# Kernel optimization log

Measured on AMD Instinct MI355X. Metric: run time of the kernel, lower is better.

## Reference

```python
import jax, jax.numpy as jnp
import numpy as np

N_NODES = 65536
N_EDGES = 524288
IN_CH = 128
HEADS = 4
HID = 16          # per-head channels (hidden_channels)
HC = HEADS * HID  # 64
EDGE_F = 8
N_GRAPHS = 512


def _glorot(key, shape):
    return jax.random.normal(key, shape, dtype=jnp.float32) / np.float32(np.sqrt(shape[0]))


def setup_inputs() -> dict:
    key = jax.random.key(0)
    ks = jax.random.split(key, 16)
    inp = {}
    inp['x'] = jax.random.normal(ks[0], (N_NODES, IN_CH), jnp.float32)
    inp['edge_attr'] = jax.random.normal(ks[1], (N_EDGES, EDGE_F), jnp.float32)
    inp['edge_index'] = jax.random.randint(ks[2], (2, N_EDGES), 0, N_NODES, dtype=jnp.int32)
    inp['batch'] = jnp.sort(jax.random.randint(ks[3], (N_NODES,), 0, N_GRAPHS, dtype=jnp.int32))
    fan1 = {'Wq1': IN_CH, 'Wk1': IN_CH, 'Wv1': IN_CH, 'We1': EDGE_F, 'Ws1': IN_CH}
    fan2 = {'Wq2': HC, 'Wk2': HC, 'Wv2': HC, 'We2': EDGE_F, 'Ws2': HC}
    i = 4
    for name, fi in {**fan1, **fan2}.items():
        inp[name] = _glorot(ks[i], (fi, HC)); i += 1
    for b in ['bq1', 'bk1', 'bv1', 'be1', 'bs1', 'bq2', 'bk2', 'bv2', 'be2', 'bs2']:
        inp[b] = jnp.zeros((HC,), jnp.float32)
    return inp


def _tconv(x, src, dst, ea, Wq, Wk, Wv, We, Ws, bq, bk, bv, be, bs):
    """PyG TransformerConv (concat=True, root_weight=True), eval mode (no dropout)."""
    n = x.shape[0]
    q = (x @ Wq + bq).reshape(n, HEADS, HID)[dst]      # [E,H,C] query at target
    k = (x @ Wk + bk).reshape(n, HEADS, HID)[src]      # [E,H,C] key from source
    v = (x @ Wv + bv).reshape(n, HEADS, HID)[src]      # [E,H,C]
    e = (ea @ We + be).reshape(-1, HEADS, HID)         # [E,H,C] edge proj
    k = k + e
    logits = (q * k).sum(-1) / np.float32(np.sqrt(HID))  # [E,H]
    m = jax.ops.segment_max(logits, dst, num_segments=n)
    m = jnp.where(jnp.isfinite(m), m, jnp.zeros_like(m))
    a = jnp.exp(logits - m[dst])
    denom = jax.ops.segment_sum(a, dst, num_segments=n)
    alpha = a / jnp.maximum(denom[dst], 1e-16)         # segment softmax over incoming edges
    msg = (v + e) * alpha[..., None]                   # [E,H,C]
    out = jax.ops.segment_sum(msg, dst, num_segments=n).reshape(n, HC)
    return out + x @ Ws + bs                           # root/skip connection


def reference(x, edge_attr, Wq1, Wk1, Wv1, We1, Ws1, bq1, bk1, bv1, be1, bs1,
              Wq2, Wk2, Wv2, We2, Ws2, bq2, bk2, bv2, be2, bs2,
              edge_index, batch):
    src, dst = edge_index[0], edge_index[1]
    h = jax.nn.relu(_tconv(x, src, dst, edge_attr,
                           Wq1, Wk1, Wv1, We1, Ws1, bq1, bk1, bv1, be1, bs1))
    h = _tconv(h, src, dst, edge_attr,
               Wq2, Wk2, Wv2, We2, Ws2, bq2, bk2, bv2, be2, bs2)
    # mean_pool_nodes: segment mean per graph
    sums = jax.ops.segment_sum(h, batch, num_segments=N_GRAPHS)
    counts = jax.ops.segment_sum(jnp.ones((h.shape[0], 1), h.dtype), batch, num_segments=N_GRAPHS)
    return sums / jnp.maximum(counts, 1.0)
```

## Files before the change

kernel.cpp:

```cpp
#include <hip/hip_runtime.h>
#include <hip/hip_bf16.h>
#include <math.h>

#define N_NODES 65536
#define N_EDGES 524288
#define IN_CH 128
#define HC 64
#define N_GRAPHS 512
#define BUCKET_CAP 64

__global__ void build_buckets(const int* __restrict__ ei, int* __restrict__ cnt,
                              int2* __restrict__ bucket) {
    int e = blockIdx.x * 256 + threadIdx.x;
    if (e >= N_EDGES) return;
    int s = ei[e];
    int d = ei[N_EDGES + e];
    int pos = atomicAdd(&cnt[d], 1);
    if (pos < BUCKET_CAP) bucket[d * BUCKET_CAP + pos] = make_int2(e, s);
}

template <int FIN>
__global__ __launch_bounds__(256) void node_gemm(
    const float* __restrict__ xin,
    const float* __restrict__ Wq, const float* __restrict__ Wk,
    const float* __restrict__ Wv, const float* __restrict__ Ws,
    const float* __restrict__ bq, const float* __restrict__ bk,
    const float* __restrict__ bv, const float* __restrict__ bs,
    float* __restrict__ q, float* __restrict__ kv,
    float* __restrict__ hout) {
    constexpr int NPB = 32;
    __shared__ float xs[NPB * FIN];
    const int c = threadIdx.x & 63;
    const int g = threadIdx.x >> 6;
    const int n0 = blockIdx.x * NPB;

    const float4* xin4 = (const float4*)(xin + (size_t)n0 * FIN);
    float4* xs4 = (float4*)xs;
    for (int i = threadIdx.x; i < NPB * FIN / 4; i += 256)
        xs4[i] = xin4[i];
    __syncthreads();

    float aq[8], ak[8], av[8], as_[8];
#pragma unroll
    for (int t = 0; t < 8; ++t) { aq[t] = 0.f; ak[t] = 0.f; av[t] = 0.f; as_[t] = 0.f; }

    for (int kk = 0; kk < FIN; ++kk) {
        float wq = Wq[kk * HC + c];
        float wk = Wk[kk * HC + c];
        float wv = Wv[kk * HC + c];
        float ws = Ws[kk * HC + c];
#pragma unroll
        for (int t = 0; t < 8; ++t) {
            float xv = xs[(g * 8 + t) * FIN + kk];
            aq[t] = fmaf(xv, wq, aq[t]);
            ak[t] = fmaf(xv, wk, ak[t]);
            av[t] = fmaf(xv, wv, av[t]);
            as_[t] = fmaf(xv, ws, as_[t]);
        }
    }
#pragma unroll
    for (int t = 0; t < 8; ++t) {
        int n = n0 + g * 8 + t;
        q[n * HC + c] = aq[t] + bq[c];
        kv[(size_t)n * 128 + c] = ak[t] + bk[c];
        kv[(size_t)n * 128 + 64 + c] = av[t] + bv[c];
        hout[n * HC + c] = as_[t] + bs[c];
    }
}

template <int RELU>
__global__ __launch_bounds__(256) void aggregate(
    const float* __restrict__ q, const float* __restrict__ kv,
    const float* __restrict__ ea,
    const float* __restrict__ We, const float* __restrict__ be,
    const int* __restrict__ cnt,
    const int2* __restrict__ bucket, float* __restrict__ hout) {
    const int wave = threadIdx.x >> 6;
    const int c = threadIdx.x & 63;
    const int n = blockIdx.x * 4 + wave;

    const float qc = q[n * HC + c] * 0.25f;
    int deg = cnt[n];
    if (deg > BUCKET_CAP) deg = BUCKET_CAP;

    int myeid = 0, mysrc = 0;
    if (c < deg) {
        int2 b = bucket[n * BUCKET_CAP + c];
        myeid = b.x;
        mysrc = b.y;
    }

    const float bec = be[c];
    float wec[8];
#pragma unroll
    for (int f = 0; f < 8; ++f) wec[f] = We[f * HC + c];

    float m = -INFINITY, d = 0.f, o = 0.f;

    float4 eA0, eA1, eB0, eB1, nA0, nA1, nB0, nB1;
    float kA, vA, kB, vB, nkA, nvA, nkB, nvB;

#define LOAD_EDGE(idx, E0, E1, KC, VC)                                   \
    {                                                                    \
        int eid_ = __builtin_amdgcn_readlane(myeid, (idx));              \
        int s_   = __builtin_amdgcn_readlane(mysrc, (idx));              \
        E0 = *(const float4*)(ea + (size_t)eid_ * 8);                    \
        E1 = *(const float4*)(ea + (size_t)eid_ * 8 + 4);                \
        KC = kv[(size_t)s_ * 128 + c];                                   \
        VC = kv[(size_t)s_ * 128 + 64 + c];                              \
    }

#define EDGE_PROJ(E0, E1, EC)                                            \
    float EC = bec;                                                      \
    EC = fmaf(E0.x, wec[0], EC); EC = fmaf(E0.y, wec[1], EC);            \
    EC = fmaf(E0.z, wec[2], EC); EC = fmaf(E0.w, wec[3], EC);            \
    EC = fmaf(E1.x, wec[4], EC); EC = fmaf(E1.y, wec[5], EC);            \
    EC = fmaf(E1.z, wec[6], EC); EC = fmaf(E1.w, wec[7], EC);

#define HEAD_REDUCE(P)                                                   \
    P += __shfl_xor(P, 1);  P += __shfl_xor(P, 2);                       \
    P += __shfl_xor(P, 4);  P += __shfl_xor(P, 8);

    const int npairs = deg >> 1;

    if (deg >= 2) {
        LOAD_EDGE(0, eA0, eA1, kA, vA);
        LOAD_EDGE(1, eB0, eB1, kB, vB);
    } else if (deg == 1) {
        LOAD_EDGE(0, eA0, eA1, kA, vA);
    }

    for (int p = 0; p < npairs; ++p) {
        int base = (p + 1) * 2;
        if (base + 1 < deg) {
            LOAD_EDGE(base, nA0, nA1, nkA, nvA);
            LOAD_EDGE(base + 1, nB0, nB1, nkB, nvB);
        } else if (base < deg) {
            LOAD_EDGE(base, nA0, nA1, nkA, nvA);
        }

        EDGE_PROJ(eA0, eA1, ecA);
        EDGE_PROJ(eB0, eB1, ecB);

        float pA = qc * (kA + ecA);
        float pB = qc * (kB + ecB);
        HEAD_REDUCE(pA);
        HEAD_REDUCE(pB);

        float newm = fmaxf(m, fmaxf(pA, pB));
        float scale = __expf(m - newm);
        float wA = __expf(pA - newm);
        float wB = __expf(pB - newm);
        d = d * scale + wA + wB;
        o = o * scale + (vA + ecA) * wA + (vB + ecB) * wB;
        m = newm;

        eA0 = nA0; eA1 = nA1; kA = nkA; vA = nvA;
        eB0 = nB0; eB1 = nB1; kB = nkB; vB = nvB;
    }

    if (deg & 1) {
        EDGE_PROJ(eA0, eA1, ecA);
        float pA = qc * (kA + ecA);
        HEAD_REDUCE(pA);
        float newm = fmaxf(m, pA);
        float scale = __expf(m - newm);
        float wA = __expf(pA - newm);
        d = d * scale + wA;
        o = o * scale + (vA + ecA) * wA;
    }

#undef LOAD_EDGE
#undef EDGE_PROJ
#undef HEAD_REDUCE

    float msg = (deg > 0) ? (o / d) : 0.f;
    float val = hout[n * HC + c] + msg;
    if (RELU) val = fmaxf(val, 0.f);
    hout[n * HC + c] = val;
}

__device__ __forceinline__ int lower_bound(const int* __restrict__ b, int val) {
    int lo = 0, hi = N_NODES;
    while (lo < hi) {
        int mid = (lo + hi) >> 1;
        if (b[mid] < val) lo = mid + 1; else hi = mid;
    }
    return lo;
}

__global__ __launch_bounds__(256) void pool_graph(const float* __restrict__ h,
                                                  const int* __restrict__ batch,
                                                  float* __restrict__ out) {
    const int g = blockIdx.x * 4 + (threadIdx.x >> 6);
    const int c = threadIdx.x & 63;
    const int s = lower_bound(batch, g);
    const int e = lower_bound(batch, g + 1);

    float a0 = 0.f, a1 = 0.f, a2 = 0.f, a3 = 0.f;
    int i = s;
    for (; i + 4 <= e; i += 4) {
        a0 += h[(size_t)i * HC + c];
        a1 += h[(size_t)(i + 1) * HC + c];
        a2 += h[(size_t)(i + 2) * HC + c];
        a3 += h[(size_t)(i + 3) * HC + c];
    }
    for (; i < e; ++i) a0 += h[(size_t)i * HC + c];
    float acc = (a0 + a1) + (a2 + a3);
    out[g * HC + c] = acc / fmaxf((float)(e - s), 1.f);
}

extern "C" void kernel_launch(void* const* d_in, const int* in_sizes, int n_in,
                              void* d_out, int out_size, void* d_ws, size_t ws_size,
                              hipStream_t stream) {
    const float* x     = (const float*)d_in[0];
    const float* ea    = (const float*)d_in[1];
    const int*   ei    = (const int*)d_in[2];
    const int*   batch = (const int*)d_in[3];
    const float* Wq1 = (const float*)d_in[4];
    const float* Wk1 = (const float*)d_in[5];
    const float* Wv1 = (const float*)d_in[6];
    const float* We1 = (const float*)d_in[7];
    const float* Ws1 = (const float*)d_in[8];
    const float* Wq2 = (const float*)d_in[9];
    const float* Wk2 = (const float*)d_in[10];
    const float* Wv2 = (const float*)d_in[11];
    const float* We2 = (const float*)d_in[12];
    const float* Ws2 = (const float*)d_in[13];
    const float* bq1 = (const float*)d_in[14];
    const float* bk1 = (const float*)d_in[15];
    const float* bv1 = (const float*)d_in[16];
    const float* be1 = (const float*)d_in[17];
    const float* bs1 = (const float*)d_in[18];
    const float* bq2 = (const float*)d_in[19];
    const float* bk2 = (const float*)d_in[20];
    const float* bv2 = (const float*)d_in[21];
    const float* be2 = (const float*)d_in[22];
    const float* bs2 = (const float*)d_in[23];
    float* out = (float*)d_out;

    char* ws = (char*)d_ws;
    size_t off = 0;
    auto alloc = [&](size_t bytes) -> void* {
        void* p = ws + off;
        off += (bytes + 255) & ~(size_t)255;
        return p;
    };
    int*   cnt    = (int*)alloc((size_t)N_NODES * 4);
    int2*  bucket = (int2*)alloc((size_t)N_NODES * BUCKET_CAP * 8);
    float* q      = (float*)alloc((size_t)N_NODES * HC * 4);
    float* kv     = (float*)alloc((size_t)N_NODES * 128 * 4);
    float* h1     = (float*)alloc((size_t)N_NODES * HC * 4);
    float* h2     = (float*)alloc((size_t)N_NODES * HC * 4);

    hipMemsetAsync(cnt, 0, (size_t)N_NODES * 4, stream);
    build_buckets<<<N_EDGES / 256, 256, 0, stream>>>(ei, cnt, bucket);

    node_gemm<IN_CH><<<N_NODES / 32, 256, 0, stream>>>(
        x, Wq1, Wk1, Wv1, Ws1, bq1, bk1, bv1, bs1, q, kv, h1);
    aggregate<1><<<N_NODES / 4, 256, 0, stream>>>(
        q, kv, ea, We1, be1, cnt, bucket, h1);

    node_gemm<HC><<<N_NODES / 32, 256, 0, stream>>>(
        h1, Wq2, Wk2, Wv2, Ws2, bq2, bk2, bv2, bs2, q, kv, h2);
    aggregate<0><<<N_NODES / 4, 256, 0, stream>>>(
        q, kv, ea, We2, be2, cnt, bucket, h2);

    pool_graph<<<N_GRAPHS / 4, 256, 0, stream>>>(h2, batch, out);
}
```

Measured before the change: 397.1 us.

## Enlarge node GEMM tile, vectorize shared loads, and double-buffer weight prefetch

The node projection kernel now handles 64 nodes per block with 16 nodes per wave instead of 32 and 8. Each wave reads x from shared memory as float4 over 4-wide K chunks, and the weight rows are loaded into registers one chunk ahead in two alternating buffers. Biases are folded into the accumulator init. The goal is more reuse of each weight load and fewer LDS instructions, at the cost of 64 accumulators per thread plus prefetch registers, which may lower occupancy or spill, and half as many blocks.

```diff
diff --git a/kernel.cpp b/kernel.cpp
--- a/kernel.cpp
+++ b/kernel.cpp
@@ -18,6 +18,37 @@
     int pos = atomicAdd(&cnt[d], 1);
     if (pos < BUCKET_CAP) bucket[d * BUCKET_CAP + pos] = make_int2(e, s);
 }
+
+#define NG_PREFETCH(CHUNK, WQ, WK, WV, WS)                                \
+    _Pragma("unroll")                                                     \
+    for (int u = 0; u < 4; ++u) {                                         \
+        WQ[u] = Wq[((CHUNK) * 4 + u) * HC + c];                           \
+        WK[u] = Wk[((CHUNK) * 4 + u) * HC + c];                           \
+        WV[u] = Wv[((CHUNK) * 4 + u) * HC + c];                           \
+        WS[u] = Ws[((CHUNK) * 4 + u) * HC + c];                           \
+    }
+
+#define NG_COMPUTE(CHUNK, WQ, WK, WV, WS)                                 \
+    _Pragma("unroll")                                                     \
+    for (int t = 0; t < NPT; ++t) {                                       \
+        float4 xv = *(const float4*)&xs[(wid * NPT + t) * FIN + (CHUNK) * 4]; \
+        aq[t] = fmaf(xv.x, WQ[0], aq[t]);                                 \
+        aq[t] = fmaf(xv.y, WQ[1], aq[t]);                                 \
+        aq[t] = fmaf(xv.z, WQ[2], aq[t]);                                 \
+        aq[t] = fmaf(xv.w, WQ[3], aq[t]);                                 \
+        ak[t] = fmaf(xv.x, WK[0], ak[t]);                                 \
+        ak[t] = fmaf(xv.y, WK[1], ak[t]);                                 \
+        ak[t] = fmaf(xv.z, WK[2], ak[t]);                                 \
+        ak[t] = fmaf(xv.w, WK[3], ak[t]);                                 \
+        av[t] = fmaf(xv.x, WV[0], av[t]);                                 \
+        av[t] = fmaf(xv.y, WV[1], av[t]);                                 \
+        av[t] = fmaf(xv.z, WV[2], av[t]);                                 \
+        av[t] = fmaf(xv.w, WV[3], av[t]);                                 \
+        as_[t] = fmaf(xv.x, WS[0], as_[t]);                               \
+        as_[t] = fmaf(xv.y, WS[1], as_[t]);                               \
+        as_[t] = fmaf(xv.z, WS[2], as_[t]);                               \
+        as_[t] = fmaf(xv.w, WS[3], as_[t]);                               \
+    }
 
 template <int FIN>
 __global__ __launch_bounds__(256) void node_gemm(
@@ -28,45 +59,53 @@
     const float* __restrict__ bv, const float* __restrict__ bs,
     float* __restrict__ q, float* __restrict__ kv,
     float* __restrict__ hout) {
-    constexpr int NPB = 32;
+    constexpr int NPB = 64;
+    constexpr int NPT = 16;
+    constexpr int NCH = FIN / 4;
     __shared__ float xs[NPB * FIN];
     const int c = threadIdx.x & 63;
-    const int g = threadIdx.x >> 6;
+    const int wid = threadIdx.x >> 6;
     const int n0 = blockIdx.x * NPB;
+
+    float wAq[4], wAk[4], wAv[4], wAs[4];
+    float wBq[4], wBk[4], wBv[4], wBs[4];
+
+    NG_PREFETCH(0, wAq, wAk, wAv, wAs)
 
     const float4* xin4 = (const float4*)(xin + (size_t)n0 * FIN);
     float4* xs4 = (float4*)xs;
     for (int i = threadIdx.x; i < NPB * FIN / 4; i += 256)
         xs4[i] = xin4[i];
+
+    float aq[NPT], ak[NPT], av[NPT], as_[NPT];
+    const float biasq = bq[c], biask = bk[c], biasv = bv[c], biass = bs[c];
+#pragma unroll
+    for (int t = 0; t < NPT; ++t) {
+        aq[t] = biasq; ak[t] = biask; av[t] = biasv; as_[t] = biass;
+    }
     __syncthreads();
 
-    float aq[8], ak[8], av[8], as_[8];
+    for (int kc = 0; kc < NCH; kc += 2) {
+        NG_PREFETCH(kc + 1, wBq, wBk, wBv, wBs)
+        NG_COMPUTE(kc, wAq, wAk, wAv, wAs)
+        if (kc + 2 < NCH) {
+            NG_PREFETCH(kc + 2, wAq, wAk, wAv, wAs)
+        }
+        NG_COMPUTE(kc + 1, wBq, wBk, wBv, wBs)
+    }
+
 #pragma unroll
-    for (int t = 0; t < 8; ++t) { aq[t] = 0.f; ak[t] = 0.f; av[t] = 0.f; as_[t] = 0.f; }
-
-    for (int kk = 0; kk < FIN; ++kk) {
-        float wq = Wq[kk * HC + c];
-        float wk = Wk[kk * HC + c];
-        float wv = Wv[kk * HC + c];
-        float ws = Ws[kk * HC + c];
-#pragma unroll
-        for (int t = 0; t < 8; ++t) {
-            float xv = xs[(g * 8 + t) * FIN + kk];
-            aq[t] = fmaf(xv, wq, aq[t]);
-            ak[t] = fmaf(xv, wk, ak[t]);
-            av[t] = fmaf(xv, wv, av[t]);
-            as_[t] = fmaf(xv, ws, as_[t]);
-        }
-    }
-#pragma unroll
-    for (int t = 0; t < 8; ++t) {
-        int n = n0 + g * 8 + t;
-        q[n * HC + c] = aq[t] + bq[c];
-        kv[(size_t)n * 128 + c] = ak[t] + bk[c];
-        kv[(size_t)n * 128 + 64 + c] = av[t] + bv[c];
-        hout[n * HC + c] = as_[t] + bs[c];
-    }
-}
+    for (int t = 0; t < NPT; ++t) {
+        int n = n0 + wid * NPT + t;
+        q[n * HC + c] = aq[t];
+        kv[(size_t)n * 128 + c] = ak[t];
+        kv[(size_t)n * 128 + 64 + c] = av[t];
+        hout[n * HC + c] = as_[t];
+    }
+}
+
+#undef NG_PREFETCH
+#undef NG_COMPUTE
 
 template <int RELU>
 __global__ __launch_bounds__(256) void aggregate(
@@ -256,12 +295,12 @@
     hipMemsetAsync(cnt, 0, (size_t)N_NODES * 4, stream);
     build_buckets<<<N_EDGES / 256, 256, 0, stream>>>(ei, cnt, bucket);
 
-    node_gemm<IN_CH><<<N_NODES / 32, 256, 0, stream>>>(
+    node_gemm<IN_CH><<<N_NODES / 64, 256, 0, stream>>>(
         x, Wq1, Wk1, Wv1, Ws1, bq1, bk1, bv1, bs1, q, kv, h1);
     aggregate<1><<<N_NODES / 4, 256, 0, stream>>>(
         q, kv, ea, We1, be1, cnt, bucket, h1);
 
-    node_gemm<HC><<<N_NODES / 32, 256, 0, stream>>>(
+    node_gemm<HC><<<N_NODES / 64, 256, 0, stream>>>(
         h1, Wq2, Wk2, Wv2, Ws2, bq2, bk2, bv2, bs2, q, kv, h2);
     aggregate<0><<<N_NODES / 4, 256, 0, stream>>>(
         q, kv, ea, We2, be2, cnt, bucket, h2);
```

Measured after the change: 390.9 us. No clear change (-1.6%).

## Remap node GEMM so each lane owns a node and 16 channels

Applied to the files above, without the earlier changes.

Restructures the node projection GEMM so each thread computes one node across 16 output channels per weight matrix, with wave-uniform weight loads (broadcast) and padded shared-memory rows for the node inputs. Blocks now cover 64 nodes, and outputs are written as float4 vectors with biases folded into accumulator init. This is meant to cut per-FMA shared-memory and global weight load traffic. In exchange it uses 64 accumulator registers per thread, which may lower occupancy, and makes the output stores strided per lane.

```diff
diff --git a/kernel.cpp b/kernel.cpp
--- a/kernel.cpp
+++ b/kernel.cpp
@@ -28,43 +28,62 @@
     const float* __restrict__ bv, const float* __restrict__ bs,
     float* __restrict__ q, float* __restrict__ kv,
     float* __restrict__ hout) {
-    constexpr int NPB = 32;
-    __shared__ float xs[NPB * FIN];
-    const int c = threadIdx.x & 63;
-    const int g = threadIdx.x >> 6;
+    constexpr int NPB = 64;
+    constexpr int PAD = 4;
+    constexpr int STRIDE = FIN + PAD;
+    __shared__ float xs[NPB * STRIDE];
+    const int lane = threadIdx.x & 63;
+    const int wid = threadIdx.x >> 6;
+    const int ch0 = wid * 16;
     const int n0 = blockIdx.x * NPB;
 
-    const float4* xin4 = (const float4*)(xin + (size_t)n0 * FIN);
-    float4* xs4 = (float4*)xs;
-    for (int i = threadIdx.x; i < NPB * FIN / 4; i += 256)
-        xs4[i] = xin4[i];
+    {
+        const float4* xin4 = (const float4*)(xin + (size_t)n0 * FIN);
+        for (int idx = threadIdx.x; idx < NPB * FIN / 4; idx += 256) {
+            int nrow = idx / (FIN / 4);
+            int c4 = idx % (FIN / 4);
+            *(float4*)&xs[nrow * STRIDE + c4 * 4] = xin4[idx];
+        }
+    }
+
+    float accq[16], acck[16], accv[16], accs[16];
+#pragma unroll
+    for (int j = 0; j < 16; ++j) {
+        accq[j] = bq[ch0 + j];
+        acck[j] = bk[ch0 + j];
+        accv[j] = bv[ch0 + j];
+        accs[j] = bs[ch0 + j];
+    }
     __syncthreads();
 
-    float aq[8], ak[8], av[8], as_[8];
-#pragma unroll
-    for (int t = 0; t < 8; ++t) { aq[t] = 0.f; ak[t] = 0.f; av[t] = 0.f; as_[t] = 0.f; }
-
+    const float* xrow = &xs[lane * STRIDE];
+#pragma unroll 2
     for (int kk = 0; kk < FIN; ++kk) {
-        float wq = Wq[kk * HC + c];
-        float wk = Wk[kk * HC + c];
-        float wv = Wv[kk * HC + c];
-        float ws = Ws[kk * HC + c];
-#pragma unroll
-        for (int t = 0; t < 8; ++t) {
-            float xv = xs[(g * 8 + t) * FIN + kk];
-            aq[t] = fmaf(xv, wq, aq[t]);
-            ak[t] = fmaf(xv, wk, ak[t]);
-            av[t] = fmaf(xv, wv, av[t]);
-            as_[t] = fmaf(xv, ws, as_[t]);
+        float xv = xrow[kk];
+        const float* wqr = Wq + kk * HC + ch0;
+        const float* wkr = Wk + kk * HC + ch0;
+        const float* wvr = Wv + kk * HC + ch0;
+        const float* wsr = Ws + kk * HC + ch0;
+#pragma unroll
+        for (int j = 0; j < 16; ++j) {
+            accq[j] = fmaf(xv, wqr[j], accq[j]);
+            acck[j] = fmaf(xv, wkr[j], acck[j]);
+            accv[j] = fmaf(xv, wvr[j], accv[j]);
+            accs[j] = fmaf(xv, wsr[j], accs[j]);
         }
     }
-#pragma unroll
-    for (int t = 0; t < 8; ++t) {
-        int n = n0 + g * 8 + t;
-        q[n * HC + c] = aq[t] + bq[c];
-        kv[(size_t)n * 128 + c] = ak[t] + bk[c];
-        kv[(size_t)n * 128 + 64 + c] = av[t] + bv[c];
-        hout[n * HC + c] = as_[t] + bs[c];
+
+    const int n = n0 + lane;
+#pragma unroll
+    for (int j4 = 0; j4 < 4; ++j4) {
+        *(float4*)&q[(size_t)n * HC + ch0 + j4 * 4] =
+            make_float4(accq[j4*4], accq[j4*4+1], accq[j4*4+2], accq[j4*4+3]);
+        *(float4*)&kv[(size_t)n * 128 + ch0 + j4 * 4] =
+            make_float4(acck[j4*4], acck[j4*4+1], acck[j4*4+2], acck[j4*4+3]);
+        *(float4*)&kv[(size_t)n * 128 + 64 + ch0 + j4 * 4] =
+            make_float4(accv[j4*4], accv[j4*4+1], accv[j4*4+2], accv[j4*4+3]);
+        *(float4*)&hout[(size_t)n * HC + ch0 + j4 * 4] =
+            make_float4(accs[j4*4], accs[j4*4+1], accs[j4*4+2], accs[j4*4+3]);
     }
 }
 
@@ -256,12 +275,12 @@
     hipMemsetAsync(cnt, 0, (size_t)N_NODES * 4, stream);
     build_buckets<<<N_EDGES / 256, 256, 0, stream>>>(ei, cnt, bucket);
 
-    node_gemm<IN_CH><<<N_NODES / 32, 256, 0, stream>>>(
+    node_gemm<IN_CH><<<N_NODES / 64, 256, 0, stream>>>(
         x, Wq1, Wk1, Wv1, Ws1, bq1, bk1, bv1, bs1, q, kv, h1);
     aggregate<1><<<N_NODES / 4, 256, 0, stream>>>(
         q, kv, ea, We1, be1, cnt, bucket, h1);
 
-    node_gemm<HC><<<N_NODES / 32, 256, 0, stream>>>(
+    node_gemm<HC><<<N_NODES / 64, 256, 0, stream>>>(
         h1, Wq2, Wk2, Wv2, Ws2, bq2, bk2, bv2, bs2, q, kv, h2);
     aggregate<0><<<N_NODES / 4, 256, 0, stream>>>(
         q, kv, ea, We2, be2, cnt, bucket, h2);
```

Result: slower. 727.1 us (+83.1%).

## Use split-bf16 MFMA for node projections and DPP for head reductions

Applied to the files above, without the earlier changes.

Replaces the scalar fp32 FMA node GEMM with a matrix-core kernel. It splits both activations and weights into bf16 hi/lo parts and sums three MFMA products (hi*hi, lo*hi, hi*lo) to get close to fp32 accuracy. A new kernel packs the weights into the MFMA fragment layout, and activations are staged into swizzled LDS. The per-head reduction in aggregate also swaps shuffle-xor for DPP row ops. The GEMM should be far cheaper, at the cost of a slight accuracy loss, more launches and heavier register use.

```diff
diff --git a/kernel.cpp b/kernel.cpp
--- a/kernel.cpp
+++ b/kernel.cpp
@@ -8,6 +8,17 @@
 #define HC 64
 #define N_GRAPHS 512
 #define BUCKET_CAP 64
+
+typedef __attribute__((ext_vector_type(8))) short short8v;
+typedef __attribute__((ext_vector_type(4))) float float4v;
+
+__device__ __forceinline__ ushort f32_to_bf16_rne(float x) {
+    unsigned u = __float_as_uint(x);
+    return (ushort)((u + 0x7fffu + ((u >> 16) & 1u)) >> 16);
+}
+__device__ __forceinline__ float bf16_to_f32(ushort h) {
+    return __uint_as_float(((unsigned)h) << 16);
+}
 
 __global__ void build_buckets(const int* __restrict__ ei, int* __restrict__ cnt,
                               int2* __restrict__ bucket) {
@@ -19,53 +30,158 @@
     if (pos < BUCKET_CAP) bucket[d * BUCKET_CAP + pos] = make_int2(e, s);
 }
 
+__global__ void pack_weights(
+    const float* __restrict__ Wq1, const float* __restrict__ Wk1,
+    const float* __restrict__ Wv1, const float* __restrict__ Ws1,
+    const float* __restrict__ Wq2, const float* __restrict__ Wk2,
+    const float* __restrict__ Wv2, const float* __restrict__ Ws2,
+    ushort* __restrict__ wf1_hi, ushort* __restrict__ wf1_lo,
+    ushort* __restrict__ wf2_hi, ushort* __restrict__ wf2_lo) {
+    int f = blockIdx.x * 256 + threadIdx.x;
+    if (f >= 6144) return;
+    const float* W;
+    ushort *ph, *pl;
+    int fl;
+    if (f < 4096) {
+        int mat = f >> 10; fl = f & 1023;
+        W = (mat == 0) ? Wq1 : (mat == 1) ? Wk1 : (mat == 2) ? Wv1 : Ws1;
+        ph = wf1_hi + (size_t)mat * 1024 * 8;
+        pl = wf1_lo + (size_t)mat * 1024 * 8;
+    } else {
+        int g = f - 4096;
+        int mat = g >> 9; fl = g & 511;
+        W = (mat == 0) ? Wq2 : (mat == 1) ? Wk2 : (mat == 2) ? Wv2 : Ws2;
+        ph = wf2_hi + (size_t)mat * 512 * 8;
+        pl = wf2_lo + (size_t)mat * 512 * 8;
+    }
+    int lane = fl & 63;
+    int ct = (fl >> 6) & 3;
+    int ks = fl >> 8;
+    int col = ct * 16 + (lane & 15);
+    int k0 = ks * 32 + (lane >> 4) * 8;
+    ushort h8[8], l8[8];
+#pragma unroll
+    for (int j = 0; j < 8; ++j) {
+        float w = W[(size_t)(k0 + j) * HC + col];
+        ushort h = f32_to_bf16_rne(w);
+        float r = w - bf16_to_f32(h);
+        h8[j] = h;
+        l8[j] = f32_to_bf16_rne(r);
+    }
+    *(uint4*)&ph[(size_t)fl * 8] = *(uint4*)h8;
+    *(uint4*)&pl[(size_t)fl * 8] = *(uint4*)l8;
+}
+
 template <int FIN>
-__global__ __launch_bounds__(256) void node_gemm(
+__global__ __launch_bounds__(256, 2) void node_gemm_mfma(
     const float* __restrict__ xin,
-    const float* __restrict__ Wq, const float* __restrict__ Wk,
-    const float* __restrict__ Wv, const float* __restrict__ Ws,
+    const ushort* __restrict__ wf_hi, const ushort* __restrict__ wf_lo,
     const float* __restrict__ bq, const float* __restrict__ bk,
     const float* __restrict__ bv, const float* __restrict__ bs,
-    float* __restrict__ q, float* __restrict__ kv,
-    float* __restrict__ hout) {
-    constexpr int NPB = 32;
-    __shared__ float xs[NPB * FIN];
-    const int c = threadIdx.x & 63;
-    const int g = threadIdx.x >> 6;
+    float* __restrict__ q, float* __restrict__ kv, float* __restrict__ hout) {
+    constexpr int NPB = 128;
+    constexpr int KS = FIN / 32;
+    constexpr int KC = FIN / 8;
+    __shared__ ushort xs[2 * NPB * KC * 8];
+    constexpr int LOHALF = NPB * KC * 8;
+    const int tid = threadIdx.x;
+    const int lane = tid & 63;
+    const int w = tid >> 6;
     const int n0 = blockIdx.x * NPB;
 
-    const float4* xin4 = (const float4*)(xin + (size_t)n0 * FIN);
-    float4* xs4 = (float4*)xs;
-    for (int i = threadIdx.x; i < NPB * FIN / 4; i += 256)
-        xs4[i] = xin4[i];
+    for (int c = tid; c < NPB * KC; c += 256) {
+        int r = c / KC, kc = c % KC;
+        const float4* src = (const float4*)(xin + (size_t)(n0 + r) * FIN + kc * 8);
+        float4 x0 = src[0], x1 = src[1];
+        float xv[8] = {x0.x, x0.y, x0.z, x0.w, x1.x, x1.y, x1.z, x1.w};
+        ushort h[8], l[8];
+#pragma unroll
+        for (int j = 0; j < 8; ++j) {
+            h[j] = f32_to_bf16_rne(xv[j]);
+            l[j] = f32_to_bf16_rne(xv[j] - bf16_to_f32(h[j]));
+        }
+        int kcs = kc ^ (r & 7);
+        *(uint4*)&xs[(size_t)(r * KC + kcs) * 8] = *(uint4*)h;
+        *(uint4*)&xs[LOHALF + (size_t)(r * KC + kcs) * 8] = *(uint4*)l;
+    }
+
+    const int ch16 = lane & 15;
+    float bqv[4], bkv[4], bvv[4], bsv[4];
+#pragma unroll
+    for (int ct = 0; ct < 4; ++ct) {
+        bqv[ct] = bq[ct * 16 + ch16];
+        bkv[ct] = bk[ct * 16 + ch16];
+        bvv[ct] = bv[ct * 16 + ch16];
+        bsv[ct] = bs[ct * 16 + ch16];
+    }
+    float4v acc[2][16];
+#pragma unroll
+    for (int t = 0; t < 16; ++t) {
+        int mat = t >> 2, ct = t & 3;
+        float b = (mat == 0) ? bqv[ct] : (mat == 1) ? bkv[ct]
+                : (mat == 2) ? bvv[ct] : bsv[ct];
+        acc[0][t] = (float4v){b, b, b, b};
+        acc[1][t] = (float4v){b, b, b, b};
+    }
     __syncthreads();
 
-    float aq[8], ak[8], av[8], as_[8];
-#pragma unroll
-    for (int t = 0; t < 8; ++t) { aq[t] = 0.f; ak[t] = 0.f; av[t] = 0.f; as_[t] = 0.f; }
-
-    for (int kk = 0; kk < FIN; ++kk) {
-        float wq = Wq[kk * HC + c];
-        float wk = Wk[kk * HC + c];
-        float wv = Wv[kk * HC + c];
-        float ws = Ws[kk * HC + c];
-#pragma unroll
-        for (int t = 0; t < 8; ++t) {
-            float xv = xs[(g * 8 + t) * FIN + kk];
-            aq[t] = fmaf(xv, wq, aq[t]);
-            ak[t] = fmaf(xv, wk, ak[t]);
-            av[t] = fmaf(xv, wv, av[t]);
-            as_[t] = fmaf(xv, ws, as_[t]);
-        }
-    }
-#pragma unroll
-    for (int t = 0; t < 8; ++t) {
-        int n = n0 + g * 8 + t;
-        q[n * HC + c] = aq[t] + bq[c];
-        kv[(size_t)n * 128 + c] = ak[t] + bk[c];
-        kv[(size_t)n * 128 + 64 + c] = av[t] + bv[c];
-        hout[n * HC + c] = as_[t] + bs[c];
-    }
+    const int g = lane >> 4;
+    for (int ks = 0; ks < KS; ++ks) {
+        short8v ah[2], al[2];
+#pragma unroll
+        for (int mt = 0; mt < 2; ++mt) {
+            int r = w * 32 + mt * 16 + (lane & 15);
+            int kcs = (ks * 4 + g) ^ (r & 7);
+            ah[mt] = *(const short8v*)&xs[(size_t)(r * KC + kcs) * 8];
+            al[mt] = *(const short8v*)&xs[LOHALF + (size_t)(r * KC + kcs) * 8];
+        }
+#pragma unroll
+        for (int t = 0; t < 16; ++t) {
+            int mat = t >> 2, ct = t & 3;
+            size_t fo = (((size_t)mat * KS * 4) + ks * 4 + ct) * 64 + lane;
+            short8v bh = *(const short8v*)&wf_hi[fo * 8];
+            short8v bl = *(const short8v*)&wf_lo[fo * 8];
+            acc[0][t] = __builtin_amdgcn_mfma_f32_16x16x32_bf16(ah[0], bh, acc[0][t], 0, 0, 0);
+            acc[1][t] = __builtin_amdgcn_mfma_f32_16x16x32_bf16(ah[1], bh, acc[1][t], 0, 0, 0);
+            acc[0][t] = __builtin_amdgcn_mfma_f32_16x16x32_bf16(al[0], bh, acc[0][t], 0, 0, 0);
+            acc[1][t] = __builtin_amdgcn_mfma_f32_16x16x32_bf16(al[1], bh, acc[1][t], 0, 0, 0);
+            acc[0][t] = __builtin_amdgcn_mfma_f32_16x16x32_bf16(ah[0], bl, acc[0][t], 0, 0, 0);
+            acc[1][t] = __builtin_amdgcn_mfma_f32_16x16x32_bf16(ah[1], bl, acc[1][t], 0, 0, 0);
+        }
+    }
+
+    const int rloc = (lane >> 4) * 4;
+#pragma unroll
+    for (int mt = 0; mt < 2; ++mt) {
+        int nbase = n0 + w * 32 + mt * 16 + rloc;
+#pragma unroll
+        for (int t = 0; t < 16; ++t) {
+            int mat = t >> 2;
+            int ch = (t & 3) * 16 + ch16;
+#pragma unroll
+            for (int r2 = 0; r2 < 4; ++r2) {
+                int n = nbase + r2;
+                float v = acc[mt][t][r2];
+                if (mat == 0)      q[(size_t)n * HC + ch] = v;
+                else if (mat == 1) kv[(size_t)n * 128 + ch] = v;
+                else if (mat == 2) kv[(size_t)n * 128 + 64 + ch] = v;
+                else               hout[(size_t)n * HC + ch] = v;
+            }
+        }
+    }
+}
+
+__device__ __forceinline__ float dpp_sum16(float x) {
+    int t;
+    t = __builtin_amdgcn_update_dpp(0, __float_as_int(x), 0xB1, 0xF, 0xF, true);
+    x += __int_as_float(t);
+    t = __builtin_amdgcn_update_dpp(0, __float_as_int(x), 0x4E, 0xF, 0xF, true);
+    x += __int_as_float(t);
+    t = __builtin_amdgcn_update_dpp(0, __float_as_int(x), 0x141, 0xF, 0xF, true);
+    x += __int_as_float(t);
+    t = __builtin_amdgcn_update_dpp(0, __float_as_int(x), 0x140, 0xF, 0xF, true);
+    x += __int_as_float(t);
+    return x;
 }
 
 template <int RELU>
@@ -117,10 +233,6 @@
     EC = fmaf(E1.x, wec[4], EC); EC = fmaf(E1.y, wec[5], EC);            \
     EC = fmaf(E1.z, wec[6], EC); EC = fmaf(E1.w, wec[7], EC);
 
-#define HEAD_REDUCE(P)                                                   \
-    P += __shfl_xor(P, 1);  P += __shfl_xor(P, 2);                       \
-    P += __shfl_xor(P, 4);  P += __shfl_xor(P, 8);
-
     const int npairs = deg >> 1;
 
     if (deg >= 2) {
@@ -142,10 +254,8 @@
         EDGE_PROJ(eA0, eA1, ecA);
         EDGE_PROJ(eB0, eB1, ecB);
 
-        float pA = qc * (kA + ecA);
-        float pB = qc * (kB + ecB);
-        HEAD_REDUCE(pA);
-        HEAD_REDUCE(pB);
+        float pA = dpp_sum16(qc * (kA + ecA));
+        float pB = dpp_sum16(qc * (kB + ecB));
 
         float newm = fmaxf(m, fmaxf(pA, pB));
         float scale = __expf(m - newm);
@@ -161,8 +271,7 @@
 
     if (deg & 1) {
         EDGE_PROJ(eA0, eA1, ecA);
-        float pA = qc * (kA + ecA);
-        HEAD_REDUCE(pA);
+        float pA = dpp_sum16(qc * (kA + ecA));
         float newm = fmaxf(m, pA);
         float scale = __expf(m - newm);
         float wA = __expf(pA - newm);
@@ -172,7 +281,6 @@
 
 #undef LOAD_EDGE
 #undef EDGE_PROJ
-#undef HEAD_REDUCE
 
     float msg = (deg > 0) ? (o / d) : 0.f;
     float val = hout[n * HC + c] + msg;
@@ -246,23 +354,29 @@
         off += (bytes + 255) & ~(size_t)255;
         return p;
     };
-    int*   cnt    = (int*)alloc((size_t)N_NODES * 4);
-    int2*  bucket = (int2*)alloc((size_t)N_NODES * BUCKET_CAP * 8);
-    float* q      = (float*)alloc((size_t)N_NODES * HC * 4);
-    float* kv     = (float*)alloc((size_t)N_NODES * 128 * 4);
-    float* h1     = (float*)alloc((size_t)N_NODES * HC * 4);
-    float* h2     = (float*)alloc((size_t)N_NODES * HC * 4);
+    int*    cnt    = (int*)alloc((size_t)N_NODES * 4);
+    int2*   bucket = (int2*)alloc((size_t)N_NODES * BUCKET_CAP * 8);
+    float*  q      = (float*)alloc((size_t)N_NODES * HC * 4);
+    float*  kv     = (float*)alloc((size_t)N_NODES * 128 * 4);
+    float*  h1     = (float*)alloc((size_t)N_NODES * HC * 4);
+    float*  h2     = (float*)alloc((size_t)N_NODES * HC * 4);
+    ushort* wf1_hi = (ushort*)alloc((size_t)4 * 1024 * 8 * 2);
+    ushort* wf1_lo = (ushort*)alloc((size_t)4 * 1024 * 8 * 2);
+    ushort* wf2_hi = (ushort*)alloc((size_t)4 * 512 * 8 * 2);
+    ushort* wf2_lo = (ushort*)alloc((size_t)4 * 512 * 8 * 2);
 
     hipMemsetAsync(cnt, 0, (size_t)N_NODES * 4, stream);
     build_buckets<<<N_EDGES / 256, 256, 0, stream>>>(ei, cnt, bucket);
-
-    node_gemm<IN_CH><<<N_NODES / 32, 256, 0, stream>>>(
-        x, Wq1, Wk1, Wv1, Ws1, bq1, bk1, bv1, bs1, q, kv, h1);
+    pack_weights<<<24, 256, 0, stream>>>(Wq1, Wk1, Wv1, Ws1, Wq2, Wk2, Wv2, Ws2,
+                                         wf1_hi, wf1_lo, wf2_hi, wf2_lo);
+
+    node_gemm_mfma<IN_CH><<<N_NODES / 128, 256, 0, stream>>>(
+        x, wf1_hi, wf1_lo, bq1, bk1, bv1, bs1, q, kv, h1);
     aggregate<1><<<N_NODES / 4, 256, 0, stream>>>(
         q, kv, ea, We1, be1, cnt, bucket, h1);
 
-    node_gemm<HC><<<N_NODES / 32, 256, 0, stream>>>(
-        h1, Wq2, Wk2, Wv2, Ws2, bq2, bk2, bv2, bs2, q, kv, h2);
+    node_gemm_mfma<HC><<<N_NODES / 128, 256, 0, stream>>>(
+        h1, wf2_hi, wf2_lo, bq2, bk2, bv2, bs2, q, kv, h2);
     aggregate<0><<<N_NODES / 4, 256, 0, stream>>>(
         q, kv, ea, We2, be2, cnt, bucket, h2);
 
```

After: 325.8 us. 1.22x faster.
